# Kernel optimization log

Measured on AMD Instinct MI355X. Metric: run time of the kernel, lower is better.

## Reference

```python
import jax, jax.numpy as jnp
import numpy as np

# e2m1 (nvfp4) representable magnitudes and rounding midpoints
E2M1_POS = jnp.array([0.0, 0.5, 1.0, 1.5, 2.0, 3.0, 4.0, 6.0], dtype=jnp.float32)
E2M1_BOUNDS = jnp.array([0.25, 0.75, 1.25, 1.75, 2.5, 3.5, 5.0], dtype=jnp.float32)
E2M1_TABLE = jnp.concatenate([E2M1_POS, -E2M1_POS])  # 4-bit code -> value (sign bit = bit 3)
BLOCK = 16  # nvfp4 block-scale group size


def _fp8_round(v):
    # simulate storage of block scales in float8 e4m3
    return v.astype(jnp.float8_e4m3fn).astype(jnp.float32)


def _e2m1_round(v):
    # round-to-nearest onto the e2m1 grid (|v| must be pre-clipped to <= 6)
    idx = jnp.searchsorted(E2M1_BOUNDS, jnp.abs(v))
    return jnp.sign(v) * E2M1_POS[idx]


def setup_inputs() -> dict:
    key = jax.random.key(0)
    k1, k2, k3, k4, k5 = jax.random.split(key, 5)
    M, H = 4096, 4096
    x = jax.random.normal(k1, (M, 2 * H), dtype=jnp.float32)
    w = jax.random.randint(k2, (H, H // 2), 0, 256, dtype=jnp.int32)  # packed fp4, 2 nibbles/byte
    wscale = jax.random.normal(k3, (H, H // BLOCK), dtype=jnp.float32)  # cast to fp8 inside
    wscale2 = jax.random.uniform(k4, (1,), dtype=jnp.float32)
    scale = jax.random.uniform(k5, (1,), dtype=jnp.float32)
    return {"x": x, "w": w, "wscale": wscale, "wscale2": wscale2, "scale": scale}


def reference(x, w, wscale, wscale2, scale):
    M = x.shape[0]
    H = x.shape[1] // 2
    # SiLU-and-mul
    y = jax.nn.silu(x[:, :H]) * x[:, H:]                 # [M, H]
    gs = 1.0 / scale[0]                                  # global input scale (1/self.scale)
    # NVFP4 dynamic quant: per-16-element block amax -> fp8 block scale, values -> e2m1
    yb = y.reshape(M, H // BLOCK, BLOCK)
    amax = jnp.max(jnp.abs(yb), axis=-1)                 # [M, H/16]
    sf = _fp8_round(amax * (gs / 6.0))                   # fp8-stored block scales
    inv = jnp.where(sf > 0, gs / sf, 0.0)
    q = _e2m1_round(jnp.clip(yb * inv[..., None], -6.0, 6.0))
    a_deq = (q * sf[..., None]).reshape(M, H)            # fp4 value * fp8 block scale
    # Weight side: unpack fp4 nibbles (low nibble = even k), dequant with fp8 block scales
    wu = w.astype(jnp.uint8)
    lo = (wu & 0xF).astype(jnp.int32)
    hi = (wu >> 4).astype(jnp.int32)
    codes = jnp.stack([lo, hi], axis=-1).reshape(H, H)   # [N, K]
    b_q = E2M1_TABLE[codes]
    ws = _fp8_round(wscale)                              # model stores wscale in fp8
    b_deq = b_q * jnp.repeat(ws, BLOCK, axis=1)          # [N, K]
    # cutlass_scaled_fp4_mm with alpha = scale * wscale2 undoing global scales
    alpha = scale[0] * wscale2[0]
    out = alpha * (a_deq @ b_deq.T)                      # [M, N]
    return out
```

## Files before the change

### kernel.cpp

```cpp
#include <hip/hip_runtime.h>
#include <math.h>

typedef unsigned int uint;
typedef unsigned short ushort;
typedef __attribute__((ext_vector_type(8))) short bf16x8;
typedef __attribute__((ext_vector_type(4))) float f32x4;

static constexpr int Mdim = 4096;
static constexpr int Ndim = 4096;
static constexpr int Kdim = 4096;
static constexpr int Hdim = 4096;


__device__ __forceinline__ float fp8_round(float v) {
  float a = fabsf(v);
  float q;
  if (a >= 0x1p-6f) {
    uint u = __float_as_uint(a);
    int e = (int)(u >> 23) - 127;
    float quant = __uint_as_float((uint)(e - 3 + 127) << 23);
    q = rintf(a / quant) * quant;
    q = fminf(q, 448.f);
  } else {
    q = rintf(a * 512.f) * 0x1p-9f;
  }
  return copysignf(q, v);
}

__device__ __forceinline__ float e2m1_round(float t) {
  float a = fabsf(t);
  float q;
  if (a <= 0.25f) q = 0.f;
  else if (a <= 0.75f) q = 0.5f;
  else if (a <= 1.25f) q = 1.f;
  else if (a <= 1.75f) q = 1.5f;
  else if (a <= 2.5f)  q = 2.f;
  else if (a <= 3.5f)  q = 3.f;
  else if (a <= 5.f)   q = 4.f;
  else                 q = 6.f;
  return copysignf(q, t);
}

__device__ __forceinline__ float e2m1_decode(uint c) {
  uint m = c & 7u;
  float v;
  if (m == 0u) v = 0.f;
  else if (m == 1u) v = 0.5f;
  else v = __uint_as_float(((126u + (m >> 1)) << 23) | ((m & 1u) << 22));
  return (c & 8u) ? -v : v;
}


__global__ void silu_quant_kernel(const float* __restrict__ x, ushort* __restrict__ a_deq,
                                  const float* __restrict__ scalep) {
  const int g = blockIdx.x * 256 + threadIdx.x;
  const int row = g >> 8;
  const int blk = g & 255;
  const float gs = 1.0f / scalep[0];
  const float c6 = gs / 6.0f;
  const float* gp = x + (size_t)row * (2 * Hdim) + blk * 16;
  const float* up = gp + Hdim;
  float y[16];
  float amax = 0.f;
#pragma unroll
  for (int i = 0; i < 4; ++i) {
    float4 gv = ((const float4*)gp)[i];
    float4 uv = ((const float4*)up)[i];
    float ga[4] = {gv.x, gv.y, gv.z, gv.w};
    float ua[4] = {uv.x, uv.y, uv.z, uv.w};
#pragma unroll
    for (int j = 0; j < 4; ++j) {
      float xv = ga[j];
      float sig = 1.0f / (1.0f + expf(-xv));
      float yy = xv * sig * ua[j];
      y[i * 4 + j] = yy;
      amax = fmaxf(amax, fabsf(yy));
    }
  }
  const float sf = fp8_round(amax * c6);
  uint outp[8];
  if (sf > 0.f) {
    const float inv = gs / sf;
#pragma unroll
    for (int i = 0; i < 8; ++i) {
      float t0 = fminf(fmaxf(y[2 * i] * inv, -6.f), 6.f);
      float t1 = fminf(fmaxf(y[2 * i + 1] * inv, -6.f), 6.f);
      float d0 = e2m1_round(t0) * sf;
      float d1 = e2m1_round(t1) * sf;
      outp[i] = (__float_as_uint(d0) >> 16) | ((__float_as_uint(d1) >> 16) << 16);
    }
  } else {
#pragma unroll
    for (int i = 0; i < 8; ++i) outp[i] = 0u;
  }
  uint4* dst = (uint4*)(a_deq + (size_t)row * Hdim + blk * 16);
  dst[0] = (uint4){outp[0], outp[1], outp[2], outp[3]};
  dst[1] = (uint4){outp[4], outp[5], outp[6], outp[7]};
}


__global__ void wdeq_kernel(const int* __restrict__ w, const float* __restrict__ wscale,
                            ushort* __restrict__ b_deq) {
  const int g = blockIdx.x * 256 + threadIdx.x;
  const int n = g >> 8;
  const int blk = g & 255;
  const int4* wp = (const int4*)(w + (size_t)n * (Hdim / 2) + blk * 8);
  int4 w0 = wp[0], w1 = wp[1];
  int wb[8] = {w0.x, w0.y, w0.z, w0.w, w1.x, w1.y, w1.z, w1.w};
  const float ws = fp8_round(wscale[(size_t)n * (Hdim / 16) + blk]);
  uint outp[8];
#pragma unroll
  for (int i = 0; i < 8; ++i) {
    uint byte = (uint)wb[i] & 0xFFu;
    float vlo = e2m1_decode(byte & 15u) * ws;
    float vhi = e2m1_decode(byte >> 4) * ws;
    outp[i] = (__float_as_uint(vlo) >> 16) | ((__float_as_uint(vhi) >> 16) << 16);
  }
  uint4* dst = (uint4*)(b_deq + (size_t)n * Hdim + blk * 16);
  dst[0] = (uint4){outp[0], outp[1], outp[2], outp[3]};
  dst[1] = (uint4){outp[4], outp[5], outp[6], outp[7]};
}


#define BM 256
#define BN 256
#define BK 64
#define NT (Kdim / BK)
#define TILE_E (256 * 64)
#define SLOT_E (2 * TILE_E)

__device__ __forceinline__ void gload_lds16(const ushort* g, ushort* l) {
  __builtin_amdgcn_global_load_lds((const __attribute__((address_space(1))) void*)g,
                                   (__attribute__((address_space(3))) void*)l,
                                   16, 0, 0);
}

__device__ __forceinline__ void stage_half(ushort* tile, const ushort* mat, int gbase,
                                           int half, int kcol, int wave, int lane) {
#pragma unroll
  for (int rr = 0; rr < 2; ++rr) {
    const int rowbase = half * 128 + rr * 64 + wave * 8;
    const int trow = rowbase + (lane >> 3);
    const int sc = (lane & 7) ^ (trow & 7);
    gload_lds16(mat + (size_t)(gbase + trow) * Kdim + kcol + sc * 8, tile + rowbase * 64);
  }
}

__device__ __forceinline__ bf16x8 lds_frag(const ushort* tile, int r, int ck) {
  return *(const bf16x8*)(tile + r * 64 + ((ck ^ (r & 7)) * 8));
}

__global__ __launch_bounds__(512, 2) void gemm256(const ushort* __restrict__ A,
                                                  const ushort* __restrict__ B,
                                                  float* __restrict__ C,
                                                  const float* __restrict__ scalep,
                                                  const float* __restrict__ wscale2p) {
  extern __shared__ __align__(16) ushort lds[];
  const int tid = threadIdx.x;
  const int wave = tid >> 6;
  const int lane = tid & 63;
  const int wm = wave >> 2;
  const int wn = wave & 3;
  const int fr = lane & 15;
  const int fq = lane >> 4;

  const int wg = blockIdx.x;
  const int swz = (wg & 7) * 32 + (wg >> 3);
  const int m0 = (swz >> 4) * BM;
  const int n0 = (swz & 15) * BN;

  f32x4 acc[8][4];
#pragma unroll
  for (int i = 0; i < 8; ++i)
#pragma unroll
    for (int j = 0; j < 4; ++j) acc[i][j] = (f32x4){0.f, 0.f, 0.f, 0.f};

  ushort* slot0 = lds;
  ushort* slot1 = lds + SLOT_E;

  stage_half(slot0, A, m0, 0, 0, wave, lane);
  stage_half(slot0, A, m0, 1, 0, wave, lane);
  stage_half(slot0 + TILE_E, B, n0, 0, 0, wave, lane);
  stage_half(slot0 + TILE_E, B, n0, 1, 0, wave, lane);
  stage_half(slot1 + TILE_E, B, n0, 0, BK, wave, lane);
  stage_half(slot1 + TILE_E, B, n0, 1, BK, wave, lane);
  asm volatile("s_waitcnt vmcnt(4)" ::: "memory");
  __builtin_amdgcn_s_barrier();

  for (int kt = 0; kt < NT; ++kt) {
    const int cur = kt & 1;
    ushort* Acur = lds + cur * SLOT_E;
    ushort* Bcur = Acur + TILE_E;
    ushort* Anext = lds + (cur ^ 1) * SLOT_E;
    const int kA = (kt + 1) * BK;
    const int kB = (kt + 2) * BK;
    const bool haveA = (kt + 1 < NT);
    const bool haveB = (kt + 2 < NT);

    bf16x8 bfr[4][2];

    {
#pragma unroll
      for (int ni = 0; ni < 4; ++ni)
#pragma unroll
        for (int kk = 0; kk < 2; ++kk)
          bfr[ni][kk] = lds_frag(Bcur, wn * 64 + ni * 16 + fr, kk * 4 + fq);
      bf16x8 af[2][2];
#pragma unroll
      for (int m2 = 0; m2 < 2; ++m2)
#pragma unroll
        for (int kk = 0; kk < 2; ++kk)
          af[m2][kk] = lds_frag(Acur, wm * 128 + m2 * 16 + fr, kk * 4 + fq);
      asm volatile("" ::: "memory");
      if (haveA) stage_half(Anext, A, m0, 0, kA, wave, lane);
      __builtin_amdgcn_s_barrier();
      asm volatile("s_waitcnt lgkmcnt(0)" ::: "memory");
      __builtin_amdgcn_s_setprio(1);
#pragma unroll
      for (int m2 = 0; m2 < 2; ++m2)
#pragma unroll
        for (int ni = 0; ni < 4; ++ni)
#pragma unroll
          for (int kk = 0; kk < 2; ++kk)
            acc[m2][ni] = __builtin_amdgcn_mfma_f32_16x16x32_bf16(af[m2][kk], bfr[ni][kk],
                                                                  acc[m2][ni], 0, 0, 0);
      __builtin_amdgcn_s_setprio(0);
      __builtin_amdgcn_s_barrier();
    }
    {
      bf16x8 af[2][2];
#pragma unroll
      for (int m2 = 0; m2 < 2; ++m2)
#pragma unroll
        for (int kk = 0; kk < 2; ++kk)
          af[m2][kk] = lds_frag(Acur, wm * 128 + (2 + m2) * 16 + fr, kk * 4 + fq);
      asm volatile("" ::: "memory");
      if (haveA) stage_half(Anext, A, m0, 1, kA, wave, lane);
      __builtin_amdgcn_s_barrier();
      asm volatile("s_waitcnt lgkmcnt(0)" ::: "memory");
      __builtin_amdgcn_s_setprio(1);
#pragma unroll
      for (int m2 = 0; m2 < 2; ++m2)
#pragma unroll
        for (int ni = 0; ni < 4; ++ni)
#pragma unroll
          for (int kk = 0; kk < 2; ++kk)
            acc[2 + m2][ni] = __builtin_amdgcn_mfma_f32_16x16x32_bf16(af[m2][kk], bfr[ni][kk],
                                                                      acc[2 + m2][ni], 0, 0, 0);
      __builtin_amdgcn_s_setprio(0);
      __builtin_amdgcn_s_barrier();
    }
    {
      bf16x8 af[2][2];
#pragma unroll
      for (int m2 = 0; m2 < 2; ++m2)
#pragma unroll
        for (int kk = 0; kk < 2; ++kk)
          af[m2][kk] = lds_frag(Acur, wm * 128 + (4 + m2) * 16 + fr, kk * 4 + fq);
      asm volatile("" ::: "memory");
      if (haveB) stage_half(Bcur, B, n0, 0, kB, wave, lane);
      __builtin_amdgcn_s_barrier();
      asm volatile("s_waitcnt lgkmcnt(0)" ::: "memory");
      __builtin_amdgcn_s_setprio(1);
#pragma unroll
      for (int m2 = 0; m2 < 2; ++m2)
#pragma unroll
        for (int ni = 0; ni < 4; ++ni)
#pragma unroll
          for (int kk = 0; kk < 2; ++kk)
            acc[4 + m2][ni] = __builtin_amdgcn_mfma_f32_16x16x32_bf16(af[m2][kk], bfr[ni][kk],
                                                                      acc[4 + m2][ni], 0, 0, 0);
      __builtin_amdgcn_s_setprio(0);
      __builtin_amdgcn_s_barrier();
    }
    {
      bf16x8 af[2][2];
#pragma unroll
      for (int m2 = 0; m2 < 2; ++m2)
#pragma unroll
        for (int kk = 0; kk < 2; ++kk)
          af[m2][kk] = lds_frag(Acur, wm * 128 + (6 + m2) * 16 + fr, kk * 4 + fq);
      asm volatile("" ::: "memory");
      if (haveB) stage_half(Bcur, B, n0, 1, kB, wave, lane);
      __builtin_amdgcn_s_barrier();
      asm volatile("s_waitcnt lgkmcnt(0)" ::: "memory");
      __builtin_amdgcn_s_setprio(1);
#pragma unroll
      for (int m2 = 0; m2 < 2; ++m2)
#pragma unroll
        for (int ni = 0; ni < 4; ++ni)
#pragma unroll
          for (int kk = 0; kk < 2; ++kk)
            acc[6 + m2][ni] = __builtin_amdgcn_mfma_f32_16x16x32_bf16(af[m2][kk], bfr[ni][kk],
                                                                      acc[6 + m2][ni], 0, 0, 0);
      __builtin_amdgcn_s_setprio(0);
      if (haveB) asm volatile("s_waitcnt vmcnt(4)" ::: "memory");
      else       asm volatile("s_waitcnt vmcnt(0)" ::: "memory");
      __builtin_amdgcn_s_barrier();
    }
  }

  const float alpha = scalep[0] * wscale2p[0];
#pragma unroll
  for (int mi = 0; mi < 8; ++mi)
#pragma unroll
    for (int ni = 0; ni < 4; ++ni) {
      const int col = n0 + wn * 64 + ni * 16 + fr;
      const int rbase = m0 + wm * 128 + mi * 16 + fq * 4;
#pragma unroll
      for (int r = 0; r < 4; ++r)
        C[(size_t)(rbase + r) * Ndim + col] = alpha * acc[mi][ni][r];
    }
}


extern "C" void kernel_launch(void* const* d_in, const int* in_sizes, int n_in,
                              void* d_out, int out_size, void* d_ws, size_t ws_size,
                              hipStream_t stream) {
  const float* x       = (const float*)d_in[0];
  const int*   w       = (const int*)d_in[1];
  const float* wscale  = (const float*)d_in[2];
  const float* wscale2 = (const float*)d_in[3];
  const float* scale   = (const float*)d_in[4];
  float* out = (float*)d_out;

  ushort* a_deq = (ushort*)d_ws;
  ushort* b_deq = a_deq + (size_t)Mdim * Kdim;

  silu_quant_kernel<<<Mdim, 256, 0, stream>>>(x, a_deq, scale);
  wdeq_kernel<<<Ndim, 256, 0, stream>>>(w, wscale, b_deq);

  hipFuncSetAttribute((const void*)gemm256, hipFuncAttributeMaxDynamicSharedMemorySize, 131072);
  gemm256<<<(Mdim / BM) * (Ndim / BN), 512, 131072, stream>>>(a_deq, b_deq, out, scale, wscale2);
}
```

Measured before the change: 166.8 us.

## Triple-buffer A tiles and prefetch next-iteration fragments in GEMM pipeline

Restructures the GEMM main loop to use three A buffers and two B buffers (160KB LDS), staging both A and B two k-tiles ahead with rotating pointers. The first A/B fragments for the next iteration are loaded at the end of the current one so the first MFMA group need not wait on LDS reads. Global offsets are precomputed once to cut address arithmetic. The larger LDS footprint may limit occupancy to one workgroup per CU despite launch_bounds(512,2).

```diff
diff --git a/kernel.cpp b/kernel.cpp
--- a/kernel.cpp
+++ b/kernel.cpp
@@ -127,7 +127,6 @@
 #define BK 64
 #define NT (Kdim / BK)
 #define TILE_E (256 * 64)
-#define SLOT_E (2 * TILE_E)
 
 __device__ __forceinline__ void gload_lds16(const ushort* g, ushort* l) {
   __builtin_amdgcn_global_load_lds((const __attribute__((address_space(1))) void*)g,
@@ -135,20 +134,12 @@
                                    16, 0, 0);
 }
 
-__device__ __forceinline__ void stage_half(ushort* tile, const ushort* mat, int gbase,
-                                           int half, int kcol, int wave, int lane) {
-#pragma unroll
-  for (int rr = 0; rr < 2; ++rr) {
-    const int rowbase = half * 128 + rr * 64 + wave * 8;
-    const int trow = rowbase + (lane >> 3);
-    const int sc = (lane & 7) ^ (trow & 7);
-    gload_lds16(mat + (size_t)(gbase + trow) * Kdim + kcol + sc * 8, tile + rowbase * 64);
-  }
-}
-
-__device__ __forceinline__ bf16x8 lds_frag(const ushort* tile, int r, int ck) {
-  return *(const bf16x8*)(tile + r * 64 + ((ck ^ (r & 7)) * 8));
-}
+#define BAR()                                   \
+  do {                                          \
+    asm volatile("" ::: "memory");              \
+    __builtin_amdgcn_s_barrier();               \
+    asm volatile("" ::: "memory");              \
+  } while (0)
 
 __global__ __launch_bounds__(512, 2) void gemm256(const ushort* __restrict__ A,
                                                   const ushort* __restrict__ B,
@@ -175,129 +166,172 @@
 #pragma unroll
     for (int j = 0; j < 4; ++j) acc[i][j] = (f32x4){0.f, 0.f, 0.f, 0.f};
 
-  ushort* slot0 = lds;
-  ushort* slot1 = lds + SLOT_E;
-
-  stage_half(slot0, A, m0, 0, 0, wave, lane);
-  stage_half(slot0, A, m0, 1, 0, wave, lane);
-  stage_half(slot0 + TILE_E, B, n0, 0, 0, wave, lane);
-  stage_half(slot0 + TILE_E, B, n0, 1, 0, wave, lane);
-  stage_half(slot1 + TILE_E, B, n0, 0, BK, wave, lane);
-  stage_half(slot1 + TILE_E, B, n0, 1, BK, wave, lane);
-  asm volatile("s_waitcnt vmcnt(4)" ::: "memory");
-  __builtin_amdgcn_s_barrier();
+  const ushort* pA0c;
+  const ushort* pA1c;
+  ushort* pA0 = lds;
+  ushort* pA1 = lds + TILE_E;
+  ushort* pA2 = lds + 2 * TILE_E;
+  ushort* pB0 = lds + 3 * TILE_E;
+  ushort* pB1 = lds + 4 * TILE_E;
+
+  int goffA[4], goffB[4], loff[4];
+#pragma unroll
+  for (int h = 0; h < 2; ++h)
+#pragma unroll
+    for (int rr = 0; rr < 2; ++rr) {
+      const int idx = h * 2 + rr;
+      const int rowb = h * 128 + rr * 64 + wave * 8;
+      const int trow = rowb + (lane >> 3);
+      const int sc = (lane & 7) ^ (trow & 7);
+      goffA[idx] = (m0 + trow) * Kdim + sc * 8;
+      goffB[idx] = (n0 + trow) * Kdim + sc * 8;
+      loff[idx] = rowb * 64;
+    }
+
+#define STAGE_A(h, kcol)                                                  \
+  do {                                                                    \
+    gload_lds16(A + (size_t)goffA[(h)*2 + 0] + (kcol), pA2 + loff[(h)*2 + 0]); \
+    gload_lds16(A + (size_t)goffA[(h)*2 + 1] + (kcol), pA2 + loff[(h)*2 + 1]); \
+  } while (0)
+#define STAGE_B(h, kcol)                                                  \
+  do {                                                                    \
+    gload_lds16(B + (size_t)goffB[(h)*2 + 0] + (kcol), pB0 + loff[(h)*2 + 0]); \
+    gload_lds16(B + (size_t)goffB[(h)*2 + 1] + (kcol), pB0 + loff[(h)*2 + 1]); \
+  } while (0)
+
+  const int laneAOff = (wm * 128 + fr) * 64;
+  const int laneBOff = (wn * 64 + fr) * 64;
+  const int xo0 = (fq ^ (fr & 7)) * 8;
+  const int xo1 = ((4 + fq) ^ (fr & 7)) * 8;
+
+  {
+    ushort* sv = pA2;
+    pA2 = pA0; STAGE_A(0, 0); STAGE_A(1, 0);
+    pB0 = pB0; STAGE_B(0, 0); STAGE_B(1, 0);
+    pA2 = pA1; STAGE_A(0, BK); STAGE_A(1, BK);
+    { ushort* t = pB0; pB0 = pB1; STAGE_B(0, BK); STAGE_B(1, BK); pB0 = t; }
+    pA2 = sv;
+  }
+  asm volatile("s_waitcnt vmcnt(8)" ::: "memory");
+  BAR();
+
+  bf16x8 af0[2][2], bfr[4][2];
+  {
+    const ushort* aR0 = pA0 + laneAOff + xo0;
+    const ushort* aR1 = pA0 + laneAOff + xo1;
+    const ushort* bR0 = pB0 + laneBOff + xo0;
+    const ushort* bR1 = pB0 + laneBOff + xo1;
+#pragma unroll
+    for (int ni = 0; ni < 4; ++ni) {
+      bfr[ni][0] = *(const bf16x8*)(bR0 + ni * 1024);
+      bfr[ni][1] = *(const bf16x8*)(bR1 + ni * 1024);
+    }
+#pragma unroll
+    for (int m2 = 0; m2 < 2; ++m2) {
+      af0[m2][0] = *(const bf16x8*)(aR0 + m2 * 1024);
+      af0[m2][1] = *(const bf16x8*)(aR1 + m2 * 1024);
+    }
+  }
 
   for (int kt = 0; kt < NT; ++kt) {
-    const int cur = kt & 1;
-    ushort* Acur = lds + cur * SLOT_E;
-    ushort* Bcur = Acur + TILE_E;
-    ushort* Anext = lds + (cur ^ 1) * SLOT_E;
-    const int kA = (kt + 1) * BK;
-    const int kB = (kt + 2) * BK;
-    const bool haveA = (kt + 1 < NT);
-    const bool haveB = (kt + 2 < NT);
-
-    bf16x8 bfr[4][2];
-
-    {
+    const int kc = (kt + 2) * BK;
+    const bool stg = (kt + 2) < NT;
+    const bool nxt = (kt + 1) < NT;
+    const ushort* aR0 = pA0 + laneAOff + xo0;
+    const ushort* aR1 = pA0 + laneAOff + xo1;
+    bf16x8 af1[2][2], af2[2][2], af3[2][2];
+
+#pragma unroll
+    for (int m2 = 0; m2 < 2; ++m2) {
+      af1[m2][0] = *(const bf16x8*)(aR0 + (2 + m2) * 1024);
+      af1[m2][1] = *(const bf16x8*)(aR1 + (2 + m2) * 1024);
+    }
+    if (stg) STAGE_A(0, kc);
+    BAR();
+    __builtin_amdgcn_s_setprio(1);
+#pragma unroll
+    for (int m2 = 0; m2 < 2; ++m2)
 #pragma unroll
       for (int ni = 0; ni < 4; ++ni)
 #pragma unroll
         for (int kk = 0; kk < 2; ++kk)
-          bfr[ni][kk] = lds_frag(Bcur, wn * 64 + ni * 16 + fr, kk * 4 + fq);
-      bf16x8 af[2][2];
-#pragma unroll
-      for (int m2 = 0; m2 < 2; ++m2)
+          acc[m2][ni] = __builtin_amdgcn_mfma_f32_16x16x32_bf16(af0[m2][kk], bfr[ni][kk],
+                                                                acc[m2][ni], 0, 0, 0);
+    __builtin_amdgcn_s_setprio(0);
+    BAR();
+
+#pragma unroll
+    for (int m2 = 0; m2 < 2; ++m2) {
+      af2[m2][0] = *(const bf16x8*)(aR0 + (4 + m2) * 1024);
+      af2[m2][1] = *(const bf16x8*)(aR1 + (4 + m2) * 1024);
+    }
+    if (stg) STAGE_A(1, kc);
+    BAR();
+    __builtin_amdgcn_s_setprio(1);
+#pragma unroll
+    for (int m2 = 0; m2 < 2; ++m2)
+#pragma unroll
+      for (int ni = 0; ni < 4; ++ni)
 #pragma unroll
         for (int kk = 0; kk < 2; ++kk)
-          af[m2][kk] = lds_frag(Acur, wm * 128 + m2 * 16 + fr, kk * 4 + fq);
-      asm volatile("" ::: "memory");
-      if (haveA) stage_half(Anext, A, m0, 0, kA, wave, lane);
-      __builtin_amdgcn_s_barrier();
-      asm volatile("s_waitcnt lgkmcnt(0)" ::: "memory");
-      __builtin_amdgcn_s_setprio(1);
-#pragma unroll
-      for (int m2 = 0; m2 < 2; ++m2)
-#pragma unroll
-        for (int ni = 0; ni < 4; ++ni)
-#pragma unroll
-          for (int kk = 0; kk < 2; ++kk)
-            acc[m2][ni] = __builtin_amdgcn_mfma_f32_16x16x32_bf16(af[m2][kk], bfr[ni][kk],
-                                                                  acc[m2][ni], 0, 0, 0);
-      __builtin_amdgcn_s_setprio(0);
-      __builtin_amdgcn_s_barrier();
-    }
-    {
-      bf16x8 af[2][2];
-#pragma unroll
-      for (int m2 = 0; m2 < 2; ++m2)
+          acc[2 + m2][ni] = __builtin_amdgcn_mfma_f32_16x16x32_bf16(af1[m2][kk], bfr[ni][kk],
+                                                                    acc[2 + m2][ni], 0, 0, 0);
+    __builtin_amdgcn_s_setprio(0);
+    BAR();
+
+#pragma unroll
+    for (int m2 = 0; m2 < 2; ++m2) {
+      af3[m2][0] = *(const bf16x8*)(aR0 + (6 + m2) * 1024);
+      af3[m2][1] = *(const bf16x8*)(aR1 + (6 + m2) * 1024);
+    }
+    if (stg) STAGE_B(0, kc);
+    BAR();
+    __builtin_amdgcn_s_setprio(1);
+#pragma unroll
+    for (int m2 = 0; m2 < 2; ++m2)
+#pragma unroll
+      for (int ni = 0; ni < 4; ++ni)
 #pragma unroll
         for (int kk = 0; kk < 2; ++kk)
-          af[m2][kk] = lds_frag(Acur, wm * 128 + (2 + m2) * 16 + fr, kk * 4 + fq);
-      asm volatile("" ::: "memory");
-      if (haveA) stage_half(Anext, A, m0, 1, kA, wave, lane);
-      __builtin_amdgcn_s_barrier();
-      asm volatile("s_waitcnt lgkmcnt(0)" ::: "memory");
-      __builtin_amdgcn_s_setprio(1);
-#pragma unroll
-      for (int m2 = 0; m2 < 2; ++m2)
-#pragma unroll
-        for (int ni = 0; ni < 4; ++ni)
-#pragma unroll
-          for (int kk = 0; kk < 2; ++kk)
-            acc[2 + m2][ni] = __builtin_amdgcn_mfma_f32_16x16x32_bf16(af[m2][kk], bfr[ni][kk],
-                                                                      acc[2 + m2][ni], 0, 0, 0);
-      __builtin_amdgcn_s_setprio(0);
-      __builtin_amdgcn_s_barrier();
-    }
-    {
-      bf16x8 af[2][2];
-#pragma unroll
-      for (int m2 = 0; m2 < 2; ++m2)
+          acc[4 + m2][ni] = __builtin_amdgcn_mfma_f32_16x16x32_bf16(af2[m2][kk], bfr[ni][kk],
+                                                                    acc[4 + m2][ni], 0, 0, 0);
+    __builtin_amdgcn_s_setprio(0);
+    if (stg) asm volatile("s_waitcnt vmcnt(6)" ::: "memory");
+    else     asm volatile("s_waitcnt vmcnt(0)" ::: "memory");
+    BAR();
+
+    if (stg) STAGE_B(1, kc);
+    BAR();
+    __builtin_amdgcn_s_setprio(1);
+#pragma unroll
+    for (int m2 = 0; m2 < 2; ++m2)
+#pragma unroll
+      for (int ni = 0; ni < 4; ++ni)
 #pragma unroll
         for (int kk = 0; kk < 2; ++kk)
-          af[m2][kk] = lds_frag(Acur, wm * 128 + (4 + m2) * 16 + fr, kk * 4 + fq);
-      asm volatile("" ::: "memory");
-      if (haveB) stage_half(Bcur, B, n0, 0, kB, wave, lane);
-      __builtin_amdgcn_s_barrier();
-      asm volatile("s_waitcnt lgkmcnt(0)" ::: "memory");
-      __builtin_amdgcn_s_setprio(1);
-#pragma unroll
-      for (int m2 = 0; m2 < 2; ++m2)
-#pragma unroll
-        for (int ni = 0; ni < 4; ++ni)
-#pragma unroll
-          for (int kk = 0; kk < 2; ++kk)
-            acc[4 + m2][ni] = __builtin_amdgcn_mfma_f32_16x16x32_bf16(af[m2][kk], bfr[ni][kk],
-                                                                      acc[4 + m2][ni], 0, 0, 0);
-      __builtin_amdgcn_s_setprio(0);
-      __builtin_amdgcn_s_barrier();
-    }
-    {
-      bf16x8 af[2][2];
-#pragma unroll
-      for (int m2 = 0; m2 < 2; ++m2)
-#pragma unroll
-        for (int kk = 0; kk < 2; ++kk)
-          af[m2][kk] = lds_frag(Acur, wm * 128 + (6 + m2) * 16 + fr, kk * 4 + fq);
-      asm volatile("" ::: "memory");
-      if (haveB) stage_half(Bcur, B, n0, 1, kB, wave, lane);
-      __builtin_amdgcn_s_barrier();
-      asm volatile("s_waitcnt lgkmcnt(0)" ::: "memory");
-      __builtin_amdgcn_s_setprio(1);
-#pragma unroll
-      for (int m2 = 0; m2 < 2; ++m2)
-#pragma unroll
-        for (int ni = 0; ni < 4; ++ni)
-#pragma unroll
-          for (int kk = 0; kk < 2; ++kk)
-            acc[6 + m2][ni] = __builtin_amdgcn_mfma_f32_16x16x32_bf16(af[m2][kk], bfr[ni][kk],
-                                                                      acc[6 + m2][ni], 0, 0, 0);
-      __builtin_amdgcn_s_setprio(0);
-      if (haveB) asm volatile("s_waitcnt vmcnt(4)" ::: "memory");
-      else       asm volatile("s_waitcnt vmcnt(0)" ::: "memory");
-      __builtin_amdgcn_s_barrier();
-    }
+          acc[6 + m2][ni] = __builtin_amdgcn_mfma_f32_16x16x32_bf16(af3[m2][kk], bfr[ni][kk],
+                                                                    acc[6 + m2][ni], 0, 0, 0);
+    __builtin_amdgcn_s_setprio(0);
+    if (nxt) {
+      const ushort* aN0 = pA1 + laneAOff + xo0;
+      const ushort* aN1 = pA1 + laneAOff + xo1;
+      const ushort* bN0 = pB1 + laneBOff + xo0;
+      const ushort* bN1 = pB1 + laneBOff + xo1;
+#pragma unroll
+      for (int ni = 0; ni < 4; ++ni) {
+        bfr[ni][0] = *(const bf16x8*)(bN0 + ni * 1024);
+        bfr[ni][1] = *(const bf16x8*)(bN1 + ni * 1024);
+      }
+#pragma unroll
+      for (int m2 = 0; m2 < 2; ++m2) {
+        af0[m2][0] = *(const bf16x8*)(aN0 + m2 * 1024);
+        af0[m2][1] = *(const bf16x8*)(aN1 + m2 * 1024);
+      }
+    }
+    BAR();
+
+    { ushort* t = pA0; pA0 = pA1; pA1 = pA2; pA2 = t; }
+    { ushort* t = pB0; pB0 = pB1; pB1 = t; }
   }
 
   const float alpha = scalep[0] * wscale2p[0];
@@ -330,6 +364,6 @@
   silu_quant_kernel<<<Mdim, 256, 0, stream>>>(x, a_deq, scale);
   wdeq_kernel<<<Ndim, 256, 0, stream>>>(w, wscale, b_deq);
 
-  hipFuncSetAttribute((const void*)gemm256, hipFuncAttributeMaxDynamicSharedMemorySize, 131072);
-  gemm256<<<(Mdim / BM) * (Ndim / BN), 512, 131072, stream>>>(a_deq, b_deq, out, scale, wscale2);
-}
+  hipFuncSetAttribute((const void*)gemm256, hipFuncAttributeMaxDynamicSharedMemorySize, 163840);
+  gemm256<<<(Mdim / BM) * (Ndim / BN), 512, 163840, stream>>>(a_deq, b_deq, out, scale, wscale2);
+}
```

Result: no change. 164.4 us (-1.4%).
